# Kernel optimization log

Hardware: AMD Instinct MI355X
Metric: run time of the kernel (lower is better)

Reference implementation:

```python
import jax, jax.numpy as jnp
import numpy as np

B, T, D, H = 256, 1024, 64, 128


def _orthogonal(key, shape):
    a = jax.random.normal(key, (max(shape), max(shape)), dtype=jnp.float32)
    q, _ = jnp.linalg.qr(a)
    return q[: shape[0], : shape[1]].astype(jnp.float32)


def setup_inputs() -> dict:
    key = jax.random.key(0)
    k0, k1, k2, k3 = jax.random.split(key, 4)
    x = jax.random.normal(k0, (B, T, D), dtype=jnp.float32)
    W_xK = _orthogonal(k1, (H, D))
    W_xz = _orthogonal(k2, (H, D))
    W_hK = _orthogonal(k3, (H, H))
    b_xK = jnp.zeros((H,), jnp.float32)
    b_xz = jnp.zeros((H,), jnp.float32)
    b_hK = jnp.zeros((H,), jnp.float32)
    return {"x": x, "W_xK": W_xK, "b_xK": b_xK, "W_xz": W_xz,
            "b_xz": b_xz, "W_hK": W_hK, "b_hK": b_hK}


def reference(x, W_xK, b_xK, W_xz, b_xz, W_hK, b_hK):
    # Precompute input projections for all timesteps (batched GEMM).
    gate_x_K = jnp.einsum('btd,hd->bth', x, W_xK) + b_xK  # [B,T,H]
    gate_x_z = jnp.einsum('btd,hd->bth', x, W_xz) + b_xz  # [B,T,H]
    z_all = jnp.tanh(gate_x_z)                             # [B,T,H]
    h0 = jnp.zeros((x.shape[0], W_hK.shape[0]), x.dtype)

    def step(h, inputs):
        gxK, z = inputs  # each [B,H]
        gate_h_K = h @ W_hK.T + b_hK
        K_gain = jax.nn.sigmoid(gxK + gate_h_K)
        h_new = jnp.tanh(h + K_gain * (z - h))
        return h_new, h_new

    # scan over time dim
    _, outs = jax.lax.scan(step, h0,
                           (jnp.swapaxes(gate_x_K, 0, 1),
                            jnp.swapaxes(z_all, 0, 1)))
    outs = jnp.swapaxes(outs, 0, 1)  # [B,T,H]
    return (outs, outs)
```

## Files before the change

kernel.cpp:

```cpp
#include <hip/hip_runtime.h>
#include <hip/hip_bf16.h>
#include <hip/hip_fp16.h>

#define NB 256
#define NT 1024
#define ND 64
#define NH 128

typedef __fp16 half8 __attribute__((ext_vector_type(8)));
typedef __fp16 half4v __attribute__((ext_vector_type(4)));
typedef __fp16 half2v __attribute__((ext_vector_type(2)));
typedef float float4v __attribute__((ext_vector_type(4)));

static __device__ __forceinline__ float fast_tanh(float v) {
    float e = __expf(2.0f * v);
    return 1.0f - 2.0f * __builtin_amdgcn_rcpf(e + 1.0f);
}

static __device__ __forceinline__ float fdot2f(half2v a, half2v b, float c) {
#if __has_builtin(__builtin_amdgcn_fdot2)
    return __builtin_amdgcn_fdot2(a, b, c, false);
#else
    return c + (float)a.x * (float)b.x + (float)a.y * (float)b.y;
#endif
}

static __device__ __forceinline__ void fast_barrier() {
    asm volatile("s_waitcnt lgkmcnt(0)\n\ts_barrier" ::: "memory");
}

static __device__ __forceinline__ float dpp_xor1_add(float x) {
#if __has_builtin(__builtin_amdgcn_mov_dpp)
    int o = __builtin_amdgcn_mov_dpp(__builtin_bit_cast(int, x), 0xB1, 0xF, 0xF, true);
    return x + __builtin_bit_cast(float, o);
#else
    return x + __shfl_xor(x, 1);
#endif
}

__global__ __launch_bounds__(256) void fused_rnn_kernel(
        const float* __restrict__ x,
        const float* __restrict__ WxK, const float* __restrict__ bxK,
        const float* __restrict__ Wxz, const float* __restrict__ bxz,
        const float* __restrict__ Whk, const float* __restrict__ bhk,
        float* __restrict__ out) {
    __shared__ __align__(16) __fp16 wsm[2][128][72];
    __shared__ __align__(16) __fp16 xsm[16][72];
    __shared__ __align__(16) __fp16 hbuf[2][128];
    __shared__ __align__(16) __fp16 gbuf[2][16][132];
    __shared__ __align__(16) __fp16 zbuf[2][16][132];

    const int tid = threadIdx.x;
    const int b = blockIdx.x;
    const int wid = tid >> 6, lane = tid & 63;
    const int l16 = lane & 15, kg = lane >> 4;
    const int j = tid >> 1, kh = tid & 1;

    #pragma unroll
    for (int mat = 0; mat < 2; ++mat) {
        const float* Wsrc = mat ? Wxz : WxK;
        const float4v* ws4 = (const float4v*)(Wsrc + (size_t)(tid >> 1) * 64 + (tid & 1) * 32);
        #pragma unroll
        for (int i = 0; i < 4; ++i) {
            float4v a = ws4[2 * i], c = ws4[2 * i + 1];
            half8 hv = {(__fp16)a.x, (__fp16)a.y, (__fp16)a.z, (__fp16)a.w,
                        (__fp16)c.x, (__fp16)c.y, (__fp16)c.z, (__fp16)c.w};
            *(half8*)&wsm[mat][tid >> 1][(tid & 1) * 32 + i * 8] = hv;
        }
    }

    half2v w[32];
    {
        const float4v* wsrc = (const float4v*)(Whk + (size_t)j * NH + kh * 64);
        #pragma unroll
        for (int i = 0; i < 16; ++i) {
            float4v wv = wsrc[i];
            w[2 * i]     = __builtin_amdgcn_cvt_pkrtz(wv.x, wv.y);
            w[2 * i + 1] = __builtin_amdgcn_cvt_pkrtz(wv.z, wv.w);
        }
    }
    const float bj = bhk[j];

    const int hc0 = (2 * wid + 0) * 16 + l16;
    const int hc1 = (2 * wid + 1) * 16 + l16;
    const float bK0 = bxK[hc0], bK1 = bxK[hc1];
    const float bz0 = bxz[hc0], bz1 = bxz[hc1];

    const float4v* xsrc = (const float4v*)(x + (size_t)b * NT * ND);

    auto proj_mfma = [&](float4v (&pacc)[2][2]) {
        #pragma unroll
        for (int n2 = 0; n2 < 2; ++n2)
            #pragma unroll
            for (int mat = 0; mat < 2; ++mat)
                pacc[n2][mat] = (float4v){0.f, 0.f, 0.f, 0.f};
        #pragma unroll
        for (int ks = 0; ks < 2; ++ks) {
            half8 af = *(const half8*)&xsm[l16][ks * 32 + kg * 8];
            #pragma unroll
            for (int n2 = 0; n2 < 2; ++n2) {
                const int nt = 2 * wid + n2;
                #pragma unroll
                for (int mat = 0; mat < 2; ++mat) {
                    half8 bf = *(const half8*)&wsm[mat][nt * 16 + l16][ks * 32 + kg * 8];
                    pacc[n2][mat] =
                        __builtin_amdgcn_mfma_f32_16x16x32_f16(af, bf, pacc[n2][mat], 0, 0, 0);
                }
            }
        }
    };
    auto proj_epilogue = [&](float4v (&pacc)[2][2], int dst) {
        #pragma unroll
        for (int n2 = 0; n2 < 2; ++n2) {
            const int col = (2 * wid + n2) * 16 + l16;
            const float bK = n2 ? bK1 : bK0;
            const float bz = n2 ? bz1 : bz0;
            #pragma unroll
            for (int r = 0; r < 4; ++r) {
                const int row = kg * 4 + r;
                gbuf[dst][row][col] = (__fp16)(pacc[n2][0][r] + bK);
                zbuf[dst][row][col] = (__fp16)fast_tanh(pacc[n2][1][r] + bz);
            }
        }
    };

    {
        float4v xg = xsrc[tid];
        if (tid < 128) hbuf[0][tid] = (__fp16)0.0f;
        __syncthreads();
        half4v hx = {(__fp16)xg.x, (__fp16)xg.y, (__fp16)xg.z, (__fp16)xg.w};
        *(half4v*)&xsm[tid >> 4][(tid & 15) * 4] = hx;
        __syncthreads();
        float4v pacc[2][2];
        proj_mfma(pacc);
        proj_epilogue(pacc, 0);
        __syncthreads();
    }

    float hn = 0.0f;
    float oreg[16];
    const size_t obase = (size_t)kh * ((size_t)NB * NT * NH)
                       + (size_t)b * NT * NH + j;

    for (int c = 0; c < 64; ++c) {
        const int cb = c & 1;
        const bool more = (c + 1 < 64);

        float4v xgn;
        if (more) xgn = xsrc[(c + 1) * 256 + tid];

        float gxv[16], zvv[16];
        #pragma unroll
        for (int s = 0; s < 16; ++s) {
            gxv[s] = (float)gbuf[cb][s][j] + bj;
            zvv[s] = (float)zbuf[cb][s][j];
        }

        float4v pacc[2][2];

        #pragma unroll
        for (int s = 0; s < 16; ++s) {
            const int t = c * 16 + s;
            const half8* hs = (const half8*)&hbuf[t & 1][kh * 64];
            float a0 = 0.f, a1 = 0.f, a2 = 0.f, a3 = 0.f;
            #pragma unroll
            for (int i = 0; i < 8; ++i) {
                half8 hv = hs[i];
                a0 = fdot2f(w[4 * i + 0], __builtin_shufflevector(hv, hv, 0, 1), a0);
                a1 = fdot2f(w[4 * i + 1], __builtin_shufflevector(hv, hv, 2, 3), a1);
                a2 = fdot2f(w[4 * i + 2], __builtin_shufflevector(hv, hv, 4, 5), a2);
                a3 = fdot2f(w[4 * i + 3], __builtin_shufflevector(hv, hv, 6, 7), a3);
            }
            const float acc = (a0 + a1) + (a2 + a3);
            const float gh = dpp_xor1_add(acc);

            const float d = zvv[s] - hn;
            const float pre = gh + gxv[s];
            const float Kg = __builtin_amdgcn_rcpf(1.0f + __expf(-pre));
            const float v = __builtin_fmaf(Kg, d, hn);
            hn = fast_tanh(v);
            oreg[s] = hn;

            if (kh == 0) hbuf[(t + 1) & 1][j] = (__fp16)hn;

            if (s == 2 && more) {
                half4v hx = {(__fp16)xgn.x, (__fp16)xgn.y, (__fp16)xgn.z, (__fp16)xgn.w};
                *(half4v*)&xsm[tid >> 4][(tid & 15) * 4] = hx;
            }
            if (s == 4 && more) proj_mfma(pacc);
            if (s == 6 && more) proj_epilogue(pacc, cb ^ 1);

            fast_barrier();
        }

        #pragma unroll
        for (int s = 0; s < 16; ++s)
            out[obase + (size_t)(c * 16 + s) * NH] = oreg[s];
    }
}

extern "C" void kernel_launch(void* const* d_in, const int* in_sizes, int n_in,
                              void* d_out, int out_size, void* d_ws, size_t ws_size,
                              hipStream_t stream) {
    (void)in_sizes; (void)n_in; (void)d_ws; (void)ws_size; (void)out_size;
    const float* x   = (const float*)d_in[0];
    const float* WxK = (const float*)d_in[1];
    const float* bxK = (const float*)d_in[2];
    const float* Wxz = (const float*)d_in[3];
    const float* bxz = (const float*)d_in[4];
    const float* Whk = (const float*)d_in[5];
    const float* bhk = (const float*)d_in[6];
    float* out = (float*)d_out;

    fused_rnn_kernel<<<256, 256, 0, stream>>>(x, WxK, bxK, Wxz, bxz, Whk, bhk, out);
}
```

Before: 584.3 us.

## Split block into recurrence and projection warp groups with 4-way hidden split

The block grows to 768 threads. 512 threads run the recurrence with each hidden unit's dot product split four ways and reduced through two DPP adds. The remaining 256 threads are a producer group that computes the next chunk's input projections with MFMA, matching the barrier count with dummy barriers. This takes projection work off the serial recurrence path and halves per-thread dot-product length, at the cost of an extra reduction step and more barrier participants per step.

```diff
diff --git a/kernel.cpp b/kernel.cpp
--- a/kernel.cpp
+++ b/kernel.cpp
@@ -38,7 +38,16 @@
 #endif
 }
 
-__global__ __launch_bounds__(256) void fused_rnn_kernel(
+static __device__ __forceinline__ float dpp_xor2_add(float x) {
+#if __has_builtin(__builtin_amdgcn_mov_dpp)
+    int o = __builtin_amdgcn_mov_dpp(__builtin_bit_cast(int, x), 0x4E, 0xF, 0xF, true);
+    return x + __builtin_bit_cast(float, o);
+#else
+    return x + __shfl_xor(x, 2);
+#endif
+}
+
+__global__ __launch_bounds__(768) void fused_rnn_kernel(
         const float* __restrict__ x,
         const float* __restrict__ WxK, const float* __restrict__ bxK,
         const float* __restrict__ Wxz, const float* __restrict__ bxz,
@@ -52,41 +61,56 @@
 
     const int tid = threadIdx.x;
     const int b = blockIdx.x;
-    const int wid = tid >> 6, lane = tid & 63;
-    const int l16 = lane & 15, kg = lane >> 4;
-    const int j = tid >> 1, kh = tid & 1;
-
-    #pragma unroll
-    for (int mat = 0; mat < 2; ++mat) {
-        const float* Wsrc = mat ? Wxz : WxK;
-        const float4v* ws4 = (const float4v*)(Wsrc + (size_t)(tid >> 1) * 64 + (tid & 1) * 32);
-        #pragma unroll
-        for (int i = 0; i < 4; ++i) {
-            float4v a = ws4[2 * i], c = ws4[2 * i + 1];
-            half8 hv = {(__fp16)a.x, (__fp16)a.y, (__fp16)a.z, (__fp16)a.w,
-                        (__fp16)c.x, (__fp16)c.y, (__fp16)c.z, (__fp16)c.w};
-            *(half8*)&wsm[mat][tid >> 1][(tid & 1) * 32 + i * 8] = hv;
-        }
-    }
-
-    half2v w[32];
-    {
-        const float4v* wsrc = (const float4v*)(Whk + (size_t)j * NH + kh * 64);
-        #pragma unroll
-        for (int i = 0; i < 16; ++i) {
+
+    const int j = tid >> 2, kh = tid & 3;
+    const int pt = tid & 255;
+    const int pwid = pt >> 6, plane = pt & 63;
+    const int pl16 = plane & 15, pkg = plane >> 4;
+
+    const float4v* xsrc = (const float4v*)(x + (size_t)b * NT * ND);
+
+    if (tid < 256) {
+        #pragma unroll
+        for (int mat = 0; mat < 2; ++mat) {
+            const float* Wsrc = mat ? Wxz : WxK;
+            const float4v* ws4 = (const float4v*)(Wsrc + (size_t)(tid >> 1) * 64 + (tid & 1) * 32);
+            #pragma unroll
+            for (int i = 0; i < 4; ++i) {
+                float4v a = ws4[2 * i], c2 = ws4[2 * i + 1];
+                half8 hv = {(__fp16)a.x, (__fp16)a.y, (__fp16)a.z, (__fp16)a.w,
+                            (__fp16)c2.x, (__fp16)c2.y, (__fp16)c2.z, (__fp16)c2.w};
+                *(half8*)&wsm[mat][tid >> 1][(tid & 1) * 32 + i * 8] = hv;
+            }
+        }
+    }
+
+    half2v w[16];
+    float bj = 0.0f;
+    float hn = 0.0f;
+    float oreg[16];
+    float4v xg;
+    float bK0 = 0.f, bK1 = 0.f, bz0 = 0.f, bz1 = 0.f;
+
+    if (tid < 512) {
+        const float4v* wsrc = (const float4v*)(Whk + (size_t)j * NH + kh * 32);
+        #pragma unroll
+        for (int i = 0; i < 8; ++i) {
             float4v wv = wsrc[i];
             w[2 * i]     = __builtin_amdgcn_cvt_pkrtz(wv.x, wv.y);
             w[2 * i + 1] = __builtin_amdgcn_cvt_pkrtz(wv.z, wv.w);
         }
-    }
-    const float bj = bhk[j];
-
-    const int hc0 = (2 * wid + 0) * 16 + l16;
-    const int hc1 = (2 * wid + 1) * 16 + l16;
-    const float bK0 = bxK[hc0], bK1 = bxK[hc1];
-    const float bz0 = bxz[hc0], bz1 = bxz[hc1];
-
-    const float4v* xsrc = (const float4v*)(x + (size_t)b * NT * ND);
+        bj = bhk[j];
+        if (tid < 128) hbuf[0][tid] = (__fp16)0.0f;
+    } else {
+        xg = xsrc[pt];
+        const int hc0 = (2 * pwid + 0) * 16 + pl16;
+        const int hc1 = (2 * pwid + 1) * 16 + pl16;
+        bK0 = bxK[hc0]; bK1 = bxK[hc1];
+        bz0 = bxz[hc0]; bz1 = bxz[hc1];
+        half4v hx = {(__fp16)xg.x, (__fp16)xg.y, (__fp16)xg.z, (__fp16)xg.w};
+        *(half4v*)&xsm[pt >> 4][(pt & 15) * 4] = hx;
+    }
+    __syncthreads();
 
     auto proj_mfma = [&](float4v (&pacc)[2][2]) {
         #pragma unroll
@@ -96,13 +120,13 @@
                 pacc[n2][mat] = (float4v){0.f, 0.f, 0.f, 0.f};
         #pragma unroll
         for (int ks = 0; ks < 2; ++ks) {
-            half8 af = *(const half8*)&xsm[l16][ks * 32 + kg * 8];
+            half8 af = *(const half8*)&xsm[pl16][ks * 32 + pkg * 8];
             #pragma unroll
             for (int n2 = 0; n2 < 2; ++n2) {
-                const int nt = 2 * wid + n2;
+                const int nt = 2 * pwid + n2;
                 #pragma unroll
                 for (int mat = 0; mat < 2; ++mat) {
-                    half8 bf = *(const half8*)&wsm[mat][nt * 16 + l16][ks * 32 + kg * 8];
+                    half8 bf = *(const half8*)&wsm[mat][nt * 16 + pl16][ks * 32 + pkg * 8];
                     pacc[n2][mat] =
                         __builtin_amdgcn_mfma_f32_16x16x32_f16(af, bf, pacc[n2][mat], 0, 0, 0);
                 }
@@ -112,90 +136,88 @@
     auto proj_epilogue = [&](float4v (&pacc)[2][2], int dst) {
         #pragma unroll
         for (int n2 = 0; n2 < 2; ++n2) {
-            const int col = (2 * wid + n2) * 16 + l16;
+            const int col = (2 * pwid + n2) * 16 + pl16;
             const float bK = n2 ? bK1 : bK0;
             const float bz = n2 ? bz1 : bz0;
             #pragma unroll
             for (int r = 0; r < 4; ++r) {
-                const int row = kg * 4 + r;
+                const int row = pkg * 4 + r;
                 gbuf[dst][row][col] = (__fp16)(pacc[n2][0][r] + bK);
                 zbuf[dst][row][col] = (__fp16)fast_tanh(pacc[n2][1][r] + bz);
             }
         }
     };
 
-    {
-        float4v xg = xsrc[tid];
-        if (tid < 128) hbuf[0][tid] = (__fp16)0.0f;
-        __syncthreads();
-        half4v hx = {(__fp16)xg.x, (__fp16)xg.y, (__fp16)xg.z, (__fp16)xg.w};
-        *(half4v*)&xsm[tid >> 4][(tid & 15) * 4] = hx;
-        __syncthreads();
+    if (tid >= 512) {
         float4v pacc[2][2];
         proj_mfma(pacc);
         proj_epilogue(pacc, 0);
-        __syncthreads();
-    }
-
-    float hn = 0.0f;
-    float oreg[16];
-    const size_t obase = (size_t)kh * ((size_t)NB * NT * NH)
+        xg = xsrc[256 + pt];
+    }
+    __syncthreads();
+
+    const size_t obase = (size_t)(kh & 1) * ((size_t)NB * NT * NH)
                        + (size_t)b * NT * NH + j;
+    const int sh = (kh >> 1) * 8;
 
     for (int c = 0; c < 64; ++c) {
         const int cb = c & 1;
-        const bool more = (c + 1 < 64);
-
-        float4v xgn;
-        if (more) xgn = xsrc[(c + 1) * 256 + tid];
-
-        float gxv[16], zvv[16];
-        #pragma unroll
-        for (int s = 0; s < 16; ++s) {
-            gxv[s] = (float)gbuf[cb][s][j] + bj;
-            zvv[s] = (float)zbuf[cb][s][j];
-        }
-
-        float4v pacc[2][2];
-
-        #pragma unroll
-        for (int s = 0; s < 16; ++s) {
-            const int t = c * 16 + s;
-            const half8* hs = (const half8*)&hbuf[t & 1][kh * 64];
-            float a0 = 0.f, a1 = 0.f, a2 = 0.f, a3 = 0.f;
-            #pragma unroll
-            for (int i = 0; i < 8; ++i) {
-                half8 hv = hs[i];
-                a0 = fdot2f(w[4 * i + 0], __builtin_shufflevector(hv, hv, 0, 1), a0);
-                a1 = fdot2f(w[4 * i + 1], __builtin_shufflevector(hv, hv, 2, 3), a1);
-                a2 = fdot2f(w[4 * i + 2], __builtin_shufflevector(hv, hv, 4, 5), a2);
-                a3 = fdot2f(w[4 * i + 3], __builtin_shufflevector(hv, hv, 6, 7), a3);
-            }
-            const float acc = (a0 + a1) + (a2 + a3);
-            const float gh = dpp_xor1_add(acc);
-
-            const float d = zvv[s] - hn;
-            const float pre = gh + gxv[s];
-            const float Kg = __builtin_amdgcn_rcpf(1.0f + __expf(-pre));
-            const float v = __builtin_fmaf(Kg, d, hn);
-            hn = fast_tanh(v);
-            oreg[s] = hn;
-
-            if (kh == 0) hbuf[(t + 1) & 1][j] = (__fp16)hn;
-
-            if (s == 2 && more) {
-                half4v hx = {(__fp16)xgn.x, (__fp16)xgn.y, (__fp16)xgn.z, (__fp16)xgn.w};
-                *(half4v*)&xsm[tid >> 4][(tid & 15) * 4] = hx;
-            }
-            if (s == 4 && more) proj_mfma(pacc);
-            if (s == 6 && more) proj_epilogue(pacc, cb ^ 1);
-
-            fast_barrier();
-        }
-
-        #pragma unroll
-        for (int s = 0; s < 16; ++s)
-            out[obase + (size_t)(c * 16 + s) * NH] = oreg[s];
+
+        if (tid < 512) {
+            float gxv[16], zvv[16];
+            #pragma unroll
+            for (int s = 0; s < 16; ++s) {
+                gxv[s] = (float)gbuf[cb][s][j] + bj;
+                zvv[s] = (float)zbuf[cb][s][j];
+            }
+
+            #pragma unroll
+            for (int s = 0; s < 16; ++s) {
+                const int t = c * 16 + s;
+                const half8* hs = (const half8*)&hbuf[t & 1][kh * 32];
+                float a0 = 0.f, a1 = 0.f, a2 = 0.f, a3 = 0.f;
+                #pragma unroll
+                for (int i = 0; i < 4; ++i) {
+                    half8 hv = hs[i];
+                    a0 = fdot2f(w[4 * i + 0], __builtin_shufflevector(hv, hv, 0, 1), a0);
+                    a1 = fdot2f(w[4 * i + 1], __builtin_shufflevector(hv, hv, 2, 3), a1);
+                    a2 = fdot2f(w[4 * i + 2], __builtin_shufflevector(hv, hv, 4, 5), a2);
+                    a3 = fdot2f(w[4 * i + 3], __builtin_shufflevector(hv, hv, 6, 7), a3);
+                }
+                const float acc = (a0 + a1) + (a2 + a3);
+                const float gh = dpp_xor2_add(dpp_xor1_add(acc));
+
+                const float d = zvv[s] - hn;
+                const float pre = gh + gxv[s];
+                const float Kg = __builtin_amdgcn_rcpf(1.0f + __expf(-pre));
+                const float v = __builtin_fmaf(Kg, d, hn);
+                hn = fast_tanh(v);
+                oreg[s] = hn;
+
+                if (kh == 0) hbuf[(t + 1) & 1][j] = (__fp16)hn;
+
+                fast_barrier();
+            }
+
+            #pragma unroll
+            for (int i = 0; i < 8; ++i)
+                out[obase + (size_t)(c * 16 + sh + i) * NH] = oreg[sh + i];
+        } else {
+            if (c + 1 < 64) {
+                half4v hx = {(__fp16)xg.x, (__fp16)xg.y, (__fp16)xg.z, (__fp16)xg.w};
+                *(half4v*)&xsm[pt >> 4][(pt & 15) * 4] = hx;
+                fast_barrier();
+                float4v pacc[2][2];
+                proj_mfma(pacc);
+                proj_epilogue(pacc, cb ^ 1);
+                if (c + 2 < 64) xg = xsrc[(size_t)(c + 2) * 256 + pt];
+                #pragma unroll
+                for (int k = 0; k < 15; ++k) fast_barrier();
+            } else {
+                #pragma unroll
+                for (int k = 0; k < 16; ++k) fast_barrier();
+            }
+        }
     }
 }
 
@@ -212,5 +234,5 @@
     const float* bhk = (const float*)d_in[6];
     float* out = (float*)d_out;
 
-    fused_rnn_kernel<<<256, 256, 0, stream>>>(x, WxK, bxK, Wxz, bxz, Whk, bhk, out);
-}
+    fused_rnn_kernel<<<256, 768, 0, stream>>>(x, WxK, bxK, Wxz, bxz, Whk, bhk, out);
+}
```

Measured after the change: 628.4 us. 1.08x slower.

## Run each batch row on one wavefront with MFMA-based recurrent matvec

Applied to the files above, without the earlier changes.

The kernel moves from a 256-thread block per batch row to a single 64-lane wavefront, which removes the per-timestep block barrier. The recurrent h·W_hK^T product now runs as 16x16x32 f16 MFMAs against a register-resident transposed weight, with h broadcast across all 16 A-rows. Only one row of each result is used, so most of the MFMA work is redundant. The input projection is now done serially between 16-step chunks by the same wave rather than overlapped inside the step loop, and x for the next chunk is prefetched into registers. The trade is to swap barrier and cross-wave sync cost for serial MFMA latency per step and lower parallelism per CU.

```diff
diff --git a/kernel.cpp b/kernel.cpp
--- a/kernel.cpp
+++ b/kernel.cpp
@@ -1,5 +1,4 @@
 #include <hip/hip_runtime.h>
-#include <hip/hip_bf16.h>
 #include <hip/hip_fp16.h>
 
 #define NB 256
@@ -8,8 +7,6 @@
 #define NH 128
 
 typedef __fp16 half8 __attribute__((ext_vector_type(8)));
-typedef __fp16 half4v __attribute__((ext_vector_type(4)));
-typedef __fp16 half2v __attribute__((ext_vector_type(2)));
 typedef float float4v __attribute__((ext_vector_type(4)));
 
 static __device__ __forceinline__ float fast_tanh(float v) {
@@ -17,185 +14,180 @@
     return 1.0f - 2.0f * __builtin_amdgcn_rcpf(e + 1.0f);
 }
 
-static __device__ __forceinline__ float fdot2f(half2v a, half2v b, float c) {
-#if __has_builtin(__builtin_amdgcn_fdot2)
-    return __builtin_amdgcn_fdot2(a, b, c, false);
-#else
-    return c + (float)a.x * (float)b.x + (float)a.y * (float)b.y;
-#endif
-}
-
-static __device__ __forceinline__ void fast_barrier() {
-    asm volatile("s_waitcnt lgkmcnt(0)\n\ts_barrier" ::: "memory");
-}
-
-static __device__ __forceinline__ float dpp_xor1_add(float x) {
-#if __has_builtin(__builtin_amdgcn_mov_dpp)
-    int o = __builtin_amdgcn_mov_dpp(__builtin_bit_cast(int, x), 0xB1, 0xF, 0xF, true);
-    return x + __builtin_bit_cast(float, o);
-#else
-    return x + __shfl_xor(x, 1);
-#endif
-}
-
-__global__ __launch_bounds__(256) void fused_rnn_kernel(
+__global__ __launch_bounds__(64, 1) void fused_rnn_wave(
         const float* __restrict__ x,
         const float* __restrict__ WxK, const float* __restrict__ bxK,
         const float* __restrict__ Wxz, const float* __restrict__ bxz,
         const float* __restrict__ Whk, const float* __restrict__ bhk,
         float* __restrict__ out) {
     __shared__ __align__(16) __fp16 wsm[2][128][72];
-    __shared__ __align__(16) __fp16 xsm[16][72];
-    __shared__ __align__(16) __fp16 hbuf[2][128];
+    __shared__ __align__(16) __fp16 hbuf[128];
     __shared__ __align__(16) __fp16 gbuf[2][16][132];
     __shared__ __align__(16) __fp16 zbuf[2][16][132];
 
     const int tid = threadIdx.x;
     const int b = blockIdx.x;
-    const int wid = tid >> 6, lane = tid & 63;
-    const int l16 = lane & 15, kg = lane >> 4;
-    const int j = tid >> 1, kh = tid & 1;
-
-    #pragma unroll
+    const int kg = tid >> 4, l16 = tid & 15;
+    const int j0 = kg * 32 + l16, j1 = j0 + 16;
+
     for (int mat = 0; mat < 2; ++mat) {
         const float* Wsrc = mat ? Wxz : WxK;
-        const float4v* ws4 = (const float4v*)(Wsrc + (size_t)(tid >> 1) * 64 + (tid & 1) * 32);
-        #pragma unroll
-        for (int i = 0; i < 4; ++i) {
-            float4v a = ws4[2 * i], c = ws4[2 * i + 1];
-            half8 hv = {(__fp16)a.x, (__fp16)a.y, (__fp16)a.z, (__fp16)a.w,
-                        (__fp16)c.x, (__fp16)c.y, (__fp16)c.z, (__fp16)c.w};
-            *(half8*)&wsm[mat][tid >> 1][(tid & 1) * 32 + i * 8] = hv;
+        for (int rr = 0; rr < 2; ++rr) {
+            const int row = tid * 2 + rr;
+            const float4v* ws4 = (const float4v*)(Wsrc + (size_t)row * 64);
+            #pragma unroll
+            for (int i = 0; i < 8; ++i) {
+                float4v a = ws4[2 * i], c = ws4[2 * i + 1];
+                half8 hv = {(__fp16)a.x, (__fp16)a.y, (__fp16)a.z, (__fp16)a.w,
+                            (__fp16)c.x, (__fp16)c.y, (__fp16)c.z, (__fp16)c.w};
+                *(half8*)&wsm[mat][row][i * 8] = hv;
+            }
         }
     }
-
-    half2v w[32];
-    {
-        const float4v* wsrc = (const float4v*)(Whk + (size_t)j * NH + kh * 64);
-        #pragma unroll
-        for (int i = 0; i < 16; ++i) {
-            float4v wv = wsrc[i];
-            w[2 * i]     = __builtin_amdgcn_cvt_pkrtz(wv.x, wv.y);
-            w[2 * i + 1] = __builtin_amdgcn_cvt_pkrtz(wv.z, wv.w);
-        }
+    hbuf[tid] = (__fp16)0.0f;
+    hbuf[tid + 64] = (__fp16)0.0f;
+
+    half8 whT[8][4];
+    #pragma unroll
+    for (int ct = 0; ct < 8; ++ct)
+        #pragma unroll
+        for (int kt = 0; kt < 4; ++kt) {
+            const float* p = Whk + (size_t)(ct * 16 + l16) * 128 + kt * 32 + kg * 8;
+            float4v u = *(const float4v*)p, v = *(const float4v*)(p + 4);
+            whT[ct][kt] = (half8){(__fp16)u.x, (__fp16)u.y, (__fp16)u.z, (__fp16)u.w,
+                                  (__fp16)v.x, (__fp16)v.y, (__fp16)v.z, (__fp16)v.w};
+        }
+
+    const float bj0 = bhk[j0], bj1 = bhk[j1];
+    float bK[8], bz[8];
+    #pragma unroll
+    for (int ct = 0; ct < 8; ++ct) {
+        bK[ct] = bxK[ct * 16 + l16];
+        bz[ct] = bxz[ct * 16 + l16];
     }
-    const float bj = bhk[j];
-
-    const int hc0 = (2 * wid + 0) * 16 + l16;
-    const int hc1 = (2 * wid + 1) * 16 + l16;
-    const float bK0 = bxK[hc0], bK1 = bxK[hc1];
-    const float bz0 = bxz[hc0], bz1 = bxz[hc1];
-
-    const float4v* xsrc = (const float4v*)(x + (size_t)b * NT * ND);
-
-    auto proj_mfma = [&](float4v (&pacc)[2][2]) {
-        #pragma unroll
-        for (int n2 = 0; n2 < 2; ++n2)
-            #pragma unroll
-            for (int mat = 0; mat < 2; ++mat)
-                pacc[n2][mat] = (float4v){0.f, 0.f, 0.f, 0.f};
-        #pragma unroll
-        for (int ks = 0; ks < 2; ++ks) {
-            half8 af = *(const half8*)&xsm[l16][ks * 32 + kg * 8];
-            #pragma unroll
-            for (int n2 = 0; n2 < 2; ++n2) {
-                const int nt = 2 * wid + n2;
+    __syncthreads();
+
+    const float* xb = x + (size_t)b * NT * ND;
+    float4v xf[4];
+
+    auto xload = [&](int c) {
+        const float* px = xb + (size_t)c * 16 * 64 + (size_t)l16 * 64;
+        #pragma unroll
+        for (int kt = 0; kt < 2; ++kt) {
+            const float* q = px + kt * 32 + kg * 8;
+            xf[2 * kt]     = *(const float4v*)q;
+            xf[2 * kt + 1] = *(const float4v*)(q + 4);
+        }
+    };
+
+    auto proj = [&](int dst) {
+        half8 ax[2];
+        #pragma unroll
+        for (int kt = 0; kt < 2; ++kt) {
+            float4v u = xf[2 * kt], v = xf[2 * kt + 1];
+            ax[kt] = (half8){(__fp16)u.x, (__fp16)u.y, (__fp16)u.z, (__fp16)u.w,
+                             (__fp16)v.x, (__fp16)v.y, (__fp16)v.z, (__fp16)v.w};
+        }
+        #pragma unroll
+        for (int mat = 0; mat < 2; ++mat) {
+            float4v pc[8];
+            #pragma unroll
+            for (int ct = 0; ct < 8; ++ct) pc[ct] = (float4v){0.f, 0.f, 0.f, 0.f};
+            #pragma unroll
+            for (int kt = 0; kt < 2; ++kt)
                 #pragma unroll
-                for (int mat = 0; mat < 2; ++mat) {
-                    half8 bf = *(const half8*)&wsm[mat][nt * 16 + l16][ks * 32 + kg * 8];
-                    pacc[n2][mat] =
-                        __builtin_amdgcn_mfma_f32_16x16x32_f16(af, bf, pacc[n2][mat], 0, 0, 0);
+                for (int ct = 0; ct < 8; ++ct) {
+                    half8 bf = *(const half8*)&wsm[mat][ct * 16 + l16][kt * 32 + kg * 8];
+                    pc[ct] = __builtin_amdgcn_mfma_f32_16x16x32_f16(ax[kt], bf, pc[ct], 0, 0, 0);
                 }
+            #pragma unroll
+            for (int ct = 0; ct < 8; ++ct) {
+                const int col = ct * 16 + l16;
+                #pragma unroll
+                for (int r = 0; r < 4; ++r) {
+                    const int row = kg * 4 + r;
+                    if (mat == 0) gbuf[dst][row][col] = (__fp16)(pc[ct][r] + bK[ct]);
+                    else          zbuf[dst][row][col] = (__fp16)fast_tanh(pc[ct][r] + bz[ct]);
+                }
             }
         }
     };
-    auto proj_epilogue = [&](float4v (&pacc)[2][2], int dst) {
-        #pragma unroll
-        for (int n2 = 0; n2 < 2; ++n2) {
-            const int col = (2 * wid + n2) * 16 + l16;
-            const float bK = n2 ? bK1 : bK0;
-            const float bz = n2 ? bz1 : bz0;
-            #pragma unroll
-            for (int r = 0; r < 4; ++r) {
-                const int row = kg * 4 + r;
-                gbuf[dst][row][col] = (__fp16)(pacc[n2][0][r] + bK);
-                zbuf[dst][row][col] = (__fp16)fast_tanh(pacc[n2][1][r] + bz);
-            }
-        }
-    };
-
-    {
-        float4v xg = xsrc[tid];
-        if (tid < 128) hbuf[0][tid] = (__fp16)0.0f;
-        __syncthreads();
-        half4v hx = {(__fp16)xg.x, (__fp16)xg.y, (__fp16)xg.z, (__fp16)xg.w};
-        *(half4v*)&xsm[tid >> 4][(tid & 15) * 4] = hx;
-        __syncthreads();
-        float4v pacc[2][2];
-        proj_mfma(pacc);
-        proj_epilogue(pacc, 0);
-        __syncthreads();
-    }
-
-    float hn = 0.0f;
-    float oreg[16];
-    const size_t obase = (size_t)kh * ((size_t)NB * NT * NH)
-                       + (size_t)b * NT * NH + j;
+
+    xload(0);
+    proj(0);
+    xload(1);
+
+    float hn0 = 0.0f, hn1 = 0.0f;
+    float oreg0[16], oreg1[16];
+    const size_t CPY = (size_t)NB * NT * NH;
+    float* o0 = out + (size_t)b * NT * NH;
 
     for (int c = 0; c < 64; ++c) {
         const int cb = c & 1;
-        const bool more = (c + 1 < 64);
-
-        float4v xgn;
-        if (more) xgn = xsrc[(c + 1) * 256 + tid];
-
-        float gxv[16], zvv[16];
+
         #pragma unroll
         for (int s = 0; s < 16; ++s) {
-            gxv[s] = (float)gbuf[cb][s][j] + bj;
-            zvv[s] = (float)zbuf[cb][s][j];
-        }
-
-        float4v pacc[2][2];
+            half8 ah[4];
+            #pragma unroll
+            for (int kt = 0; kt < 4; ++kt)
+                ah[kt] = *(const half8*)&hbuf[kt * 32 + kg * 8];
+            const float g0 = (float)gbuf[cb][s][j0];
+            const float g1 = (float)gbuf[cb][s][j1];
+            const float z0 = (float)zbuf[cb][s][j0];
+            const float z1 = (float)zbuf[cb][s][j1];
+
+            float4v accA[8], accB[8];
+            #pragma unroll
+            for (int ct = 0; ct < 8; ++ct) {
+                accA[ct] = (float4v){0.f, 0.f, 0.f, 0.f};
+                accB[ct] = (float4v){0.f, 0.f, 0.f, 0.f};
+            }
+            #pragma unroll
+            for (int ct = 0; ct < 8; ++ct) {
+                accA[ct] = __builtin_amdgcn_mfma_f32_16x16x32_f16(ah[0], whT[ct][0], accA[ct], 0, 0, 0);
+                accB[ct] = __builtin_amdgcn_mfma_f32_16x16x32_f16(ah[2], whT[ct][2], accB[ct], 0, 0, 0);
+            }
+            #pragma unroll
+            for (int ct = 0; ct < 8; ++ct) {
+                accA[ct] = __builtin_amdgcn_mfma_f32_16x16x32_f16(ah[1], whT[ct][1], accA[ct], 0, 0, 0);
+                accB[ct] = __builtin_amdgcn_mfma_f32_16x16x32_f16(ah[3], whT[ct][3], accB[ct], 0, 0, 0);
+            }
+
+            const float ya0 = kg < 2 ? (kg == 0 ? accA[0][0] : accA[2][0])
+                                     : (kg == 2 ? accA[4][0] : accA[6][0]);
+            const float yb0 = kg < 2 ? (kg == 0 ? accB[0][0] : accB[2][0])
+                                     : (kg == 2 ? accB[4][0] : accB[6][0]);
+            const float ya1 = kg < 2 ? (kg == 0 ? accA[1][0] : accA[3][0])
+                                     : (kg == 2 ? accA[5][0] : accA[7][0]);
+            const float yb1 = kg < 2 ? (kg == 0 ? accB[1][0] : accB[3][0])
+                                     : (kg == 2 ? accB[5][0] : accB[7][0]);
+
+            const float pre0 = (ya0 + yb0) + (g0 + bj0);
+            const float pre1 = (ya1 + yb1) + (g1 + bj1);
+            const float K0 = __builtin_amdgcn_rcpf(1.0f + __expf(-pre0));
+            const float K1 = __builtin_amdgcn_rcpf(1.0f + __expf(-pre1));
+            hn0 = fast_tanh(__builtin_fmaf(K0, z0 - hn0, hn0));
+            hn1 = fast_tanh(__builtin_fmaf(K1, z1 - hn1, hn1));
+
+            hbuf[j0] = (__fp16)hn0;
+            hbuf[j1] = (__fp16)hn1;
+
+            oreg0[s] = hn0;
+            oreg1[s] = hn1;
+        }
+
+        if (c < 63) proj(cb ^ 1);
 
         #pragma unroll
         for (int s = 0; s < 16; ++s) {
-            const int t = c * 16 + s;
-            const half8* hs = (const half8*)&hbuf[t & 1][kh * 64];
-            float a0 = 0.f, a1 = 0.f, a2 = 0.f, a3 = 0.f;
-            #pragma unroll
-            for (int i = 0; i < 8; ++i) {
-                half8 hv = hs[i];
-                a0 = fdot2f(w[4 * i + 0], __builtin_shufflevector(hv, hv, 0, 1), a0);
-                a1 = fdot2f(w[4 * i + 1], __builtin_shufflevector(hv, hv, 2, 3), a1);
-                a2 = fdot2f(w[4 * i + 2], __builtin_shufflevector(hv, hv, 4, 5), a2);
-                a3 = fdot2f(w[4 * i + 3], __builtin_shufflevector(hv, hv, 6, 7), a3);
-            }
-            const float acc = (a0 + a1) + (a2 + a3);
-            const float gh = dpp_xor1_add(acc);
-
-            const float d = zvv[s] - hn;
-            const float pre = gh + gxv[s];
-            const float Kg = __builtin_amdgcn_rcpf(1.0f + __expf(-pre));
-            const float v = __builtin_fmaf(Kg, d, hn);
-            hn = fast_tanh(v);
-            oreg[s] = hn;
-
-            if (kh == 0) hbuf[(t + 1) & 1][j] = (__fp16)hn;
-
-            if (s == 2 && more) {
-                half4v hx = {(__fp16)xgn.x, (__fp16)xgn.y, (__fp16)xgn.z, (__fp16)xgn.w};
-                *(half4v*)&xsm[tid >> 4][(tid & 15) * 4] = hx;
-            }
-            if (s == 4 && more) proj_mfma(pacc);
-            if (s == 6 && more) proj_epilogue(pacc, cb ^ 1);
-
-            fast_barrier();
-        }
-
-        #pragma unroll
-        for (int s = 0; s < 16; ++s)
-            out[obase + (size_t)(c * 16 + s) * NH] = oreg[s];
+            float* po = o0 + (size_t)(c * 16 + s) * NH;
+            po[j0] = oreg0[s];
+            po[j1] = oreg1[s];
+            po[CPY + j0] = oreg0[s];
+            po[CPY + j1] = oreg1[s];
+        }
+
+        if (c < 62) xload(c + 2);
     }
 }
 
@@ -212,5 +204,5 @@
     const float* bhk = (const float*)d_in[6];
     float* out = (float*)d_out;
 
-    fused_rnn_kernel<<<256, 256, 0, stream>>>(x, WxK, bxK, Wxz, bxz, Whk, bhk, out);
+    fused_rnn_wave<<<256, 64, 0, stream>>>(x, WxK, bxK, Wxz, bxz, Whk, bhk, out);
 }
```

New measurement: 750.9 us. 28.5% more time.
